# Optimization experiments

Measured on AMD Instinct MI355X. Metric: run time of the kernel, lower is better.

## Reference

```python
import jax, jax.numpy as jnp
import numpy as np


def setup_inputs() -> dict:
    key = jax.random.key(0)
    ks = jax.random.split(key, 5)
    B, S, D = 2, 2048, 1024
    inv = 1.0 / np.sqrt(D)
    inp = {
        "x": jax.random.normal(ks[0], (B, S, D), jnp.float32),
        "Wq": jax.random.normal(ks[1], (D, D), jnp.float32) * inv,
        "bq": jnp.zeros((D,), jnp.float32),
        "Wk": jax.random.normal(ks[2], (D, D), jnp.float32) * inv,
        "bk": jnp.zeros((D,), jnp.float32),
        "Wv": jax.random.normal(ks[3], (D, D), jnp.float32) * inv,
        "bv": jnp.zeros((D,), jnp.float32),
        "Wo": jax.random.normal(ks[4], (D, D), jnp.float32) * inv,
        "bo": jnp.zeros((D,), jnp.float32),
        "num_heads": 16,
        "window_size": 128,
    }
    return inp


def reference(x, Wq, bq, Wk, bk, Wv, bv, Wo, bo, num_heads, window_size):
    B, S, D = x.shape
    H = num_heads
    hd = D // H
    scale = 1.0 / np.sqrt(hd)

    def split_heads(t):  # [B,S,D] -> [B,H,S,hd]
        return t.reshape(B, S, H, hd).transpose(0, 2, 1, 3)

    q = split_heads(x @ Wq + bq)
    k = split_heads(x @ Wk + bk)
    v = split_heads(x @ Wv + bv)

    # dense scores, then sliding-window + causal mask (faithful to original)
    scores = jnp.einsum('bhqd,bhkd->bhqk', q, k) * scale  # [B,H,S,S]
    i = jnp.arange(S)[:, None]
    j = jnp.arange(S)[None, :]
    # position i attends to j in [i - window_size + 1, i]
    mask = (j <= i) & (j > i - window_size)
    scores = jnp.where(mask, scores, -jnp.inf)
    attn_weights = jax.nn.softmax(scores, axis=-1)  # dropout is identity in eval

    out = jnp.einsum('bhqk,bhkd->bhqd', attn_weights, v)  # [B,H,S,hd]
    out = out.transpose(0, 2, 1, 3).reshape(B, S, D)
    return out @ Wo + bo, attn_weights
```

## Files before the change

kernel.cpp:

```cpp
#include <hip/hip_runtime.h>
#include <cmath>

typedef __attribute__((ext_vector_type(8))) __bf16 v8bf;
typedef __attribute__((ext_vector_type(4))) float  v4f;

#define DEV static __device__ __forceinline__

DEV unsigned short f2bf(float f) {
  unsigned u = __builtin_bit_cast(unsigned, f);
  unsigned r = u + 0x7fffu + ((u >> 16) & 1u);
  return (unsigned short)(r >> 16);
}
DEV float bf2f(unsigned short s) {
  return __builtin_bit_cast(float, ((unsigned)s) << 16);
}
DEV v8bf ld8(const unsigned short* p) { return *(const v8bf*)p; }

DEV void gl16(const unsigned short* g, unsigned short* l) {
  __builtin_amdgcn_global_load_lds(
      (const __attribute__((address_space(1))) unsigned int*)g,
      (__attribute__((address_space(3))) unsigned int*)l, 16, 0, 0);
}

__global__ __launch_bounds__(256) void k_cvt_x(const float* __restrict__ x,
                                               unsigned short* __restrict__ xb) {
  int i = blockIdx.x * 256 + threadIdx.x;
  float4 v = ((const float4*)x)[i];
  unsigned lo = (unsigned)f2bf(v.x) | ((unsigned)f2bf(v.y) << 16);
  unsigned hi = (unsigned)f2bf(v.z) | ((unsigned)f2bf(v.w) << 16);
  ((uint2*)xb)[i] = make_uint2(lo, hi);
}

__global__ __launch_bounds__(256) void k_trans_w4(const float* __restrict__ Wq,
                                                  const float* __restrict__ Wk,
                                                  const float* __restrict__ Wv,
                                                  const float* __restrict__ Wo,
                                                  unsigned short* __restrict__ WT,
                                                  unsigned short* __restrict__ WoT) {
  __shared__ float t[32][33];
  int z = blockIdx.z;
  const float* src = (z == 0) ? Wq : (z == 1) ? Wk : (z == 2) ? Wv : Wo;
  unsigned short* dst = (z < 3) ? WT + z * 1048576 : WoT;
  int n0 = blockIdx.x * 32, k0 = blockIdx.y * 32;
  int tx = threadIdx.x & 31, ty = threadIdx.x >> 5;
  for (int r = ty; r < 32; r += 8)
    t[r][tx] = src[(k0 + r) * 1024 + n0 + tx];
  __syncthreads();
  for (int r = ty; r < 32; r += 8)
    dst[(n0 + r) * 1024 + k0 + tx] = f2bf(t[tx][r]);
}

__global__ __launch_bounds__(256) void k_bias(const float* __restrict__ bq,
                                              const float* __restrict__ bk,
                                              const float* __restrict__ bv,
                                              float* __restrict__ dst) {
  int i = blockIdx.x * 256 + threadIdx.x;
  float v = (i < 1024) ? bq[i] : (i < 2048 ? bk[i - 1024] : bv[i - 2048]);
  dst[i] = v;
}

template <bool OUT_F32>
__global__ __launch_bounds__(256) void k_gemm(const unsigned short* __restrict__ A,
                                              const unsigned short* __restrict__ Bt,
                                              const float* __restrict__ bias,
                                              void* __restrict__ Cout,
                                              int ldc) {
  constexpr int K = 1024;
  __shared__ __attribute__((aligned(16))) unsigned short As[128 * 32];
  __shared__ __attribute__((aligned(16))) unsigned short Bs[128 * 32];
  int tid = threadIdx.x;
  int wave = tid >> 6, lane = tid & 63;
  int m0 = blockIdx.y * 128, n0 = blockIdx.x * 128;
  int wm = (wave >> 1) * 64, wn = (wave & 1) * 64;
  int m = lane & 15, q4 = lane >> 4;
  int arow = tid >> 2, acol = (tid & 3) * 8;
  v4f acc[4][4] = {};
  const unsigned short* ga0 = A + (m0 + arow) * K + acol;
  const unsigned short* ga1 = A + (m0 + 64 + arow) * K + acol;
  const unsigned short* gb0 = Bt + (n0 + arow) * K + acol;
  const unsigned short* gb1 = Bt + (n0 + 64 + arow) * K + acol;
  unsigned short* lA0 = As + wave * 512;
  unsigned short* lA1 = As + 2048 + wave * 512;
  unsigned short* lB0 = Bs + wave * 512;
  unsigned short* lB1 = Bs + 2048 + wave * 512;

  for (int kt = 0; kt < K; kt += 32) {
    gl16(ga0 + kt, lA0);
    gl16(ga1 + kt, lA1);
    gl16(gb0 + kt, lB0);
    gl16(gb1 + kt, lB1);
    __syncthreads();
    v8bf af[4], bfv[4];
#pragma unroll
    for (int mt = 0; mt < 4; mt++) af[mt] = ld8(&As[(wm + mt * 16 + m) * 32 + q4 * 8]);
#pragma unroll
    for (int nt = 0; nt < 4; nt++) bfv[nt] = ld8(&Bs[(wn + nt * 16 + m) * 32 + q4 * 8]);
#pragma unroll
    for (int mt = 0; mt < 4; mt++)
#pragma unroll
      for (int nt = 0; nt < 4; nt++)
        acc[mt][nt] = __builtin_amdgcn_mfma_f32_16x16x32_bf16(af[mt], bfv[nt], acc[mt][nt], 0, 0, 0);
    __syncthreads();
  }
#pragma unroll
  for (int mt = 0; mt < 4; mt++)
#pragma unroll
    for (int nt = 0; nt < 4; nt++) {
      int col = n0 + wn + nt * 16 + m;
      float bb = bias[col];
#pragma unroll
      for (int r = 0; r < 4; r++) {
        int row = m0 + wm + mt * 16 + q4 * 4 + r;
        float v = acc[mt][nt][r] + bb;
        if (OUT_F32) ((float*)Cout)[row * ldc + col] = v;
        else ((unsigned short*)Cout)[row * ldc + col] = f2bf(v);
      }
    }
}

__global__ __launch_bounds__(256) void k_attn(const unsigned short* __restrict__ QKV,
                                              unsigned short* __restrict__ Oatt,
                                              unsigned short* __restrict__ cb) {
  constexpr int VTS = 208;
  constexpr int PSS = 168;
  __shared__ __attribute__((aligned(16))) unsigned short Vt[64 * VTS];
  __shared__ __attribute__((aligned(16))) unsigned short Ps[4][16 * PSS];
  int b = blockIdx.z, h = blockIdx.y, i0 = blockIdx.x * 64;
  int tid = threadIdx.x, wave = tid >> 6, lane = tid & 63;
  int kbase = i0 - 128;
  const int ld = 3072;
  const unsigned short* Qg = QKV + b * 2048 * ld + h * 64;
  const unsigned short* Kg = Qg + 1024;
  const unsigned short* Vg = Qg + 2048;

  for (int c = tid; c < 192 * 16; c += 256) {
    int jl = c & 15, rest = c >> 4;
    int d0 = (rest & 15) * 4;
    int j = (rest >> 4) * 16 + jl;
    int jg = kbase + j; jg = jg < 0 ? 0 : jg;
    uint2 v = *(const uint2*)(Vg + jg * ld + d0);
    Vt[(d0 + 0) * VTS + j] = (unsigned short)(v.x & 0xffffu);
    Vt[(d0 + 1) * VTS + j] = (unsigned short)(v.x >> 16);
    Vt[(d0 + 2) * VTS + j] = (unsigned short)(v.y & 0xffffu);
    Vt[(d0 + 3) * VTS + j] = (unsigned short)(v.y >> 16);
  }
  for (int c = tid; c < 64 * 16; c += 256)
    Vt[(c >> 4) * VTS + 192 + (c & 15)] = 0;
  for (int c = lane; c < 16 * 24; c += 64)
    Ps[wave][(c / 24) * PSS + 144 + (c % 24)] = 0;
  __syncthreads();

  int qb = i0 + wave * 16;
  int m = lane & 15, q4 = lane >> 4;

  const unsigned short* qrow = Qg + (qb + m) * ld;
  v8bf qa0 = ld8(qrow + q4 * 8);
  v8bf qa1 = ld8(qrow + 32 + q4 * 8);

  v4f sc[9];
#pragma unroll
  for (int n = 0; n < 9; n++) {
    int key = kbase + wave * 16 + n * 16 + m;
    int kg = key < 0 ? 0 : key;
    const unsigned short* krow = Kg + kg * ld;
    v8bf kb0 = ld8(krow + q4 * 8);
    v8bf kb1 = ld8(krow + 32 + q4 * 8);
    v4f z = {0.f, 0.f, 0.f, 0.f};
    z = __builtin_amdgcn_mfma_f32_16x16x32_bf16(qa0, kb0, z, 0, 0, 0);
    z = __builtin_amdgcn_mfma_f32_16x16x32_bf16(qa1, kb1, z, 0, 0, 0);
    sc[n] = z;
  }
  float mx[4] = {-3e38f, -3e38f, -3e38f, -3e38f};
#pragma unroll
  for (int n = 0; n < 9; n++)
#pragma unroll
    for (int r = 0; r < 4; r++) {
      int i = qb + q4 * 4 + r;
      int j = kbase + wave * 16 + n * 16 + m;
      float v = sc[n][r] * 0.125f;
      bool ok = (j >= 0) && (j <= i) && (j > i - 128);
      v = ok ? v : -3e38f;
      sc[n][r] = v;
      mx[r] = fmaxf(mx[r], v);
    }
#pragma unroll
  for (int o = 1; o < 16; o <<= 1)
#pragma unroll
    for (int r = 0; r < 4; r++) mx[r] = fmaxf(mx[r], __shfl_xor(mx[r], o, 64));
  float sum[4] = {0.f, 0.f, 0.f, 0.f};
#pragma unroll
  for (int n = 0; n < 9; n++)
#pragma unroll
    for (int r = 0; r < 4; r++) {
      float p = __expf(sc[n][r] - mx[r]);
      sc[n][r] = p;
      sum[r] += p;
    }
#pragma unroll
  for (int o = 1; o < 16; o <<= 1)
#pragma unroll
    for (int r = 0; r < 4; r++) sum[r] += __shfl_xor(sum[r], o, 64);
  float inv[4];
#pragma unroll
  for (int r = 0; r < 4; r++) inv[r] = 1.0f / sum[r];

#pragma unroll
  for (int n = 0; n < 9; n++)
#pragma unroll
    for (int r = 0; r < 4; r++)
      Ps[wave][(q4 * 4 + r) * PSS + n * 16 + m] = f2bf(sc[n][r] * inv[r]);
  __syncthreads();

  v4f oacc[4] = {};
#pragma unroll
  for (int c = 0; c < 5; c++) {
    v8bf pa = ld8(&Ps[wave][m * PSS + c * 32 + q4 * 8]);
#pragma unroll
    for (int dt = 0; dt < 4; dt++) {
      v8bf vb = ld8(&Vt[(dt * 16 + m) * VTS + wave * 16 + c * 32 + q4 * 8]);
      oacc[dt] = __builtin_amdgcn_mfma_f32_16x16x32_bf16(pa, vb, oacc[dt], 0, 0, 0);
    }
  }
#pragma unroll
  for (int dt = 0; dt < 4; dt++)
#pragma unroll
    for (int r = 0; r < 4; r++)
      Oatt[(b * 2048 + qb + q4 * 4 + r) * 1024 + h * 64 + dt * 16 + m] = f2bf(oacc[dt][r]);

  for (int R = 0; R < 16; R++) {
    int row = (b * 16 + h) * 2048 + qb + R;
    unsigned short p0 = Ps[wave][R * PSS + R + 1 + lane * 2];
    unsigned short p1 = Ps[wave][R * PSS + R + 2 + lane * 2];
    ((unsigned*)cb)[row * 64 + lane] = (unsigned)p0 | ((unsigned)p1 << 16);
  }
}

__global__ __launch_bounds__(256) void k_wwrite(const unsigned short* __restrict__ cb,
                                                float* __restrict__ wout) {
  int tid = threadIdx.x, wave = tid >> 6, lane = tid & 63;
  int rbase = blockIdx.x * 16 + wave * 4;
  for (int rr = 0; rr < 4; rr++) {
    int row = rbase + rr;
    int i = row & 2047;
    float* rowp = wout + (size_t)row * 2048;
    const unsigned short* crow = cb + (size_t)row * 128;
    int lo = i - 127;
#pragma unroll
    for (int it = 0; it < 8; it++) {
      int col = it * 256 + lane * 4;
      float4 v = {0.f, 0.f, 0.f, 0.f};
      if (col <= i && col + 3 >= lo) {
#pragma unroll
        for (int e = 0; e < 4; e++) {
          int j = col + e;
          if (j >= lo && j <= i && j >= 0)
            (&v.x)[e] = bf2f(crow[j - lo]);
        }
      }
      *(float4*)(rowp + col) = v;
    }
  }
}

extern "C" void kernel_launch(void* const* d_in, const int* in_sizes, int n_in,
                              void* d_out, int out_size, void* d_ws, size_t ws_size,
                              hipStream_t stream) {
  (void)in_sizes; (void)n_in; (void)out_size; (void)ws_size;
  const float* x  = (const float*)d_in[0];
  const float* Wq = (const float*)d_in[1];
  const float* bq = (const float*)d_in[2];
  const float* Wk = (const float*)d_in[3];
  const float* bk = (const float*)d_in[4];
  const float* Wv = (const float*)d_in[5];
  const float* bv = (const float*)d_in[6];
  const float* Wo = (const float*)d_in[7];
  const float* bo = (const float*)d_in[8];

  char* ws = (char*)d_ws;
  unsigned short* xb   = (unsigned short*)(ws);
  unsigned short* WT   = (unsigned short*)(ws + 8388608);
  unsigned short* WoT  = (unsigned short*)(ws + 14680064);
  float*          bqkv = (float*)(ws + 16777216);
  unsigned short* QKV  = (unsigned short*)(ws + 16789504);
  unsigned short* Oat  = (unsigned short*)(ws + 41955328);
  unsigned short* cb   = (unsigned short*)(ws + 50343936);

  float* out  = (float*)d_out;
  float* wout = out + 4194304;

  k_cvt_x<<<4096, 256, 0, stream>>>(x, xb);
  k_trans_w4<<<dim3(32, 32, 4), 256, 0, stream>>>(Wq, Wk, Wv, Wo, WT, WoT);
  k_bias<<<12, 256, 0, stream>>>(bq, bk, bv, bqkv);
  k_gemm<false><<<dim3(24, 32), 256, 0, stream>>>(xb, WT, bqkv, QKV, 3072);
  k_attn<<<dim3(32, 16, 2), 256, 0, stream>>>(QKV, Oat, cb);
  k_wwrite<<<4096, 256, 0, stream>>>(cb, wout);
  k_gemm<true><<<dim3(8, 32), 256, 0, stream>>>(Oat, WoT, bo, out, 1024);
}
```

Before: 686.5 us.

## Merge prep kernels, pretranspose V globally, fuse out-proj GEMM with weight write

Folds the three preprocessing kernels into one launch and merges the output-projection GEMM with the attention-weights expansion kernel, so those independent jobs share one grid. Adds a separate kernel that transposes V into a global head-major buffer, letting the attention kernel fill its shared V tile with 16-byte vector loads instead of scattered 2-byte stores. Weight-matrix stores become nontemporal. The cost is an extra pass over V through global memory and an extra launch for the transpose.

```diff
diff --git a/kernel.cpp b/kernel.cpp
--- a/kernel.cpp
+++ b/kernel.cpp
@@ -22,49 +22,49 @@
       (__attribute__((address_space(3))) unsigned int*)l, 16, 0, 0);
 }
 
-__global__ __launch_bounds__(256) void k_cvt_x(const float* __restrict__ x,
-                                               unsigned short* __restrict__ xb) {
-  int i = blockIdx.x * 256 + threadIdx.x;
-  float4 v = ((const float4*)x)[i];
-  unsigned lo = (unsigned)f2bf(v.x) | ((unsigned)f2bf(v.y) << 16);
-  unsigned hi = (unsigned)f2bf(v.z) | ((unsigned)f2bf(v.w) << 16);
-  ((uint2*)xb)[i] = make_uint2(lo, hi);
-}
-
-__global__ __launch_bounds__(256) void k_trans_w4(const float* __restrict__ Wq,
-                                                  const float* __restrict__ Wk,
-                                                  const float* __restrict__ Wv,
-                                                  const float* __restrict__ Wo,
-                                                  unsigned short* __restrict__ WT,
-                                                  unsigned short* __restrict__ WoT) {
-  __shared__ float t[32][33];
-  int z = blockIdx.z;
-  const float* src = (z == 0) ? Wq : (z == 1) ? Wk : (z == 2) ? Wv : Wo;
-  unsigned short* dst = (z < 3) ? WT + z * 1048576 : WoT;
-  int n0 = blockIdx.x * 32, k0 = blockIdx.y * 32;
-  int tx = threadIdx.x & 31, ty = threadIdx.x >> 5;
-  for (int r = ty; r < 32; r += 8)
-    t[r][tx] = src[(k0 + r) * 1024 + n0 + tx];
-  __syncthreads();
-  for (int r = ty; r < 32; r += 8)
-    dst[(n0 + r) * 1024 + k0 + tx] = f2bf(t[tx][r]);
-}
-
-__global__ __launch_bounds__(256) void k_bias(const float* __restrict__ bq,
+__global__ __launch_bounds__(256) void k_prep(const float* __restrict__ x,
+                                              const float* __restrict__ Wq,
+                                              const float* __restrict__ Wk,
+                                              const float* __restrict__ Wv,
+                                              const float* __restrict__ Wo,
+                                              const float* __restrict__ bq,
                                               const float* __restrict__ bk,
                                               const float* __restrict__ bv,
-                                              float* __restrict__ dst) {
-  int i = blockIdx.x * 256 + threadIdx.x;
-  float v = (i < 1024) ? bq[i] : (i < 2048 ? bk[i - 1024] : bv[i - 2048]);
-  dst[i] = v;
-}
-
-template <bool OUT_F32>
-__global__ __launch_bounds__(256) void k_gemm(const unsigned short* __restrict__ A,
-                                              const unsigned short* __restrict__ Bt,
-                                              const float* __restrict__ bias,
-                                              void* __restrict__ Cout,
-                                              int ldc) {
+                                              unsigned short* __restrict__ xb,
+                                              unsigned short* __restrict__ WT,
+                                              unsigned short* __restrict__ WoT,
+                                              float* __restrict__ bqkv) {
+  __shared__ float t[32][33];
+  int bx = blockIdx.x, tid = threadIdx.x;
+  if (bx < 4096) {
+    int i = bx * 256 + tid;
+    float4 v = ((const float4*)x)[i];
+    unsigned lo = (unsigned)f2bf(v.x) | ((unsigned)f2bf(v.y) << 16);
+    unsigned hi = (unsigned)f2bf(v.z) | ((unsigned)f2bf(v.w) << 16);
+    ((uint2*)xb)[i] = make_uint2(lo, hi);
+  } else if (bx < 8192) {
+    int rem = bx - 4096;
+    int z = rem >> 10, r2 = rem & 1023;
+    const float* src = (z == 0) ? Wq : (z == 1) ? Wk : (z == 2) ? Wv : Wo;
+    unsigned short* dst = (z < 3) ? WT + z * 1048576 : WoT;
+    int n0 = (r2 & 31) * 32, k0 = (r2 >> 5) * 32;
+    int tx = tid & 31, ty = tid >> 5;
+    for (int r = ty; r < 32; r += 8)
+      t[r][tx] = src[(k0 + r) * 1024 + n0 + tx];
+    __syncthreads();
+    for (int r = ty; r < 32; r += 8)
+      dst[(n0 + r) * 1024 + k0 + tx] = f2bf(t[tx][r]);
+  } else {
+    int i = (bx - 8192) * 256 + tid;
+    float v = (i < 1024) ? bq[i] : (i < 2048 ? bk[i - 1024] : bv[i - 2048]);
+    bqkv[i] = v;
+  }
+}
+
+__global__ __launch_bounds__(256) void k_gemm1(const unsigned short* __restrict__ A,
+                                               const unsigned short* __restrict__ Bt,
+                                               const float* __restrict__ bias,
+                                               unsigned short* __restrict__ Cout) {
   constexpr int K = 1024;
   __shared__ __attribute__((aligned(16))) unsigned short As[128 * 32];
   __shared__ __attribute__((aligned(16))) unsigned short Bs[128 * 32];
@@ -111,14 +111,30 @@
 #pragma unroll
       for (int r = 0; r < 4; r++) {
         int row = m0 + wm + mt * 16 + q4 * 4 + r;
-        float v = acc[mt][nt][r] + bb;
-        if (OUT_F32) ((float*)Cout)[row * ldc + col] = v;
-        else ((unsigned short*)Cout)[row * ldc + col] = f2bf(v);
+        Cout[row * 3072 + col] = f2bf(acc[mt][nt][r] + bb);
       }
     }
 }
 
+__global__ __launch_bounds__(256) void k_transv(const unsigned short* __restrict__ QKV,
+                                                unsigned short* __restrict__ Vtg) {
+  __shared__ unsigned short t[32][33];
+  int bx = blockIdx.x, tid = threadIdx.x;
+  int st = bx & 63, h2 = (bx >> 6) & 1, bh = bx >> 7;
+  int b = bh >> 4, h = bh & 15;
+  int s0 = st * 32, d0 = h2 * 32;
+  int tx = tid & 31, ty = tid >> 5;
+  const unsigned short* src = QKV + (size_t)b * 2048 * 3072 + 2048 + h * 64 + d0;
+  for (int r = ty; r < 32; r += 8)
+    t[r][tx] = src[(size_t)(s0 + r) * 3072 + tx];
+  __syncthreads();
+  unsigned short* dst = Vtg + (size_t)(bh * 64 + d0) * 2048 + s0;
+  for (int r = ty; r < 32; r += 8)
+    dst[(size_t)r * 2048 + tx] = t[tx][r];
+}
+
 __global__ __launch_bounds__(256) void k_attn(const unsigned short* __restrict__ QKV,
+                                              const unsigned short* __restrict__ Vtg,
                                               unsigned short* __restrict__ Oatt,
                                               unsigned short* __restrict__ cb) {
   constexpr int VTS = 208;
@@ -131,21 +147,19 @@
   const int ld = 3072;
   const unsigned short* Qg = QKV + b * 2048 * ld + h * 64;
   const unsigned short* Kg = Qg + 1024;
-  const unsigned short* Vg = Qg + 2048;
-
-  for (int c = tid; c < 192 * 16; c += 256) {
-    int jl = c & 15, rest = c >> 4;
-    int d0 = (rest & 15) * 4;
-    int j = (rest >> 4) * 16 + jl;
-    int jg = kbase + j; jg = jg < 0 ? 0 : jg;
-    uint2 v = *(const uint2*)(Vg + jg * ld + d0);
-    Vt[(d0 + 0) * VTS + j] = (unsigned short)(v.x & 0xffffu);
-    Vt[(d0 + 1) * VTS + j] = (unsigned short)(v.x >> 16);
-    Vt[(d0 + 2) * VTS + j] = (unsigned short)(v.y & 0xffffu);
-    Vt[(d0 + 3) * VTS + j] = (unsigned short)(v.y >> 16);
-  }
-  for (int c = tid; c < 64 * 16; c += 256)
-    Vt[(c >> 4) * VTS + 192 + (c & 15)] = 0;
+
+  const unsigned short* vsrc = Vtg + (size_t)(b * 16 + h) * 64 * 2048;
+  for (int idx = tid; idx < 1536; idx += 256) {
+    int row = idx / 24, c16 = idx % 24;
+    int gcol = kbase + c16 * 8;
+    if (gcol < 0) gcol = 0;
+    v8bf vv = ld8(vsrc + (size_t)row * 2048 + gcol);
+    *(v8bf*)&Vt[row * VTS + c16 * 8] = vv;
+  }
+  {
+    int row = tid >> 2, c4 = (tid & 3) * 4;
+    *(uint2*)&Vt[row * VTS + 192 + c4] = make_uint2(0u, 0u);
+  }
   for (int c = lane; c < 16 * 24; c += 64)
     Ps[wave][(c / 24) * PSS + 144 + (c % 24)] = 0;
   __syncthreads();
@@ -235,29 +249,85 @@
   }
 }
 
-__global__ __launch_bounds__(256) void k_wwrite(const unsigned short* __restrict__ cb,
-                                                float* __restrict__ wout) {
+__global__ __launch_bounds__(256) void k_tail(const unsigned short* __restrict__ Oat,
+                                              const unsigned short* __restrict__ WoT,
+                                              const float* __restrict__ bo,
+                                              float* __restrict__ out,
+                                              const unsigned short* __restrict__ cb,
+                                              float* __restrict__ wout) {
+  __shared__ __attribute__((aligned(16))) unsigned short As[128 * 32];
+  __shared__ __attribute__((aligned(16))) unsigned short Bs[128 * 32];
   int tid = threadIdx.x, wave = tid >> 6, lane = tid & 63;
-  int rbase = blockIdx.x * 16 + wave * 4;
-  for (int rr = 0; rr < 4; rr++) {
-    int row = rbase + rr;
-    int i = row & 2047;
-    float* rowp = wout + (size_t)row * 2048;
-    const unsigned short* crow = cb + (size_t)row * 128;
-    int lo = i - 127;
-#pragma unroll
-    for (int it = 0; it < 8; it++) {
-      int col = it * 256 + lane * 4;
-      float4 v = {0.f, 0.f, 0.f, 0.f};
-      if (col <= i && col + 3 >= lo) {
-#pragma unroll
-        for (int e = 0; e < 4; e++) {
-          int j = col + e;
-          if (j >= lo && j <= i && j >= 0)
-            (&v.x)[e] = bf2f(crow[j - lo]);
+
+  if (blockIdx.x < 256) {
+    constexpr int K = 1024;
+    int bx = blockIdx.x;
+    int n0 = (bx & 7) * 128, m0 = (bx >> 3) * 128;
+    int wm = (wave >> 1) * 64, wn = (wave & 1) * 64;
+    int m = lane & 15, q4 = lane >> 4;
+    int arow = tid >> 2, acol = (tid & 3) * 8;
+    v4f acc[4][4] = {};
+    const unsigned short* ga0 = Oat + (m0 + arow) * K + acol;
+    const unsigned short* ga1 = Oat + (m0 + 64 + arow) * K + acol;
+    const unsigned short* gb0 = WoT + (n0 + arow) * K + acol;
+    const unsigned short* gb1 = WoT + (n0 + 64 + arow) * K + acol;
+    unsigned short* lA0 = As + wave * 512;
+    unsigned short* lA1 = As + 2048 + wave * 512;
+    unsigned short* lB0 = Bs + wave * 512;
+    unsigned short* lB1 = Bs + 2048 + wave * 512;
+    for (int kt = 0; kt < K; kt += 32) {
+      gl16(ga0 + kt, lA0);
+      gl16(ga1 + kt, lA1);
+      gl16(gb0 + kt, lB0);
+      gl16(gb1 + kt, lB1);
+      __syncthreads();
+      v8bf af[4], bfv[4];
+#pragma unroll
+      for (int mt = 0; mt < 4; mt++) af[mt] = ld8(&As[(wm + mt * 16 + m) * 32 + q4 * 8]);
+#pragma unroll
+      for (int nt = 0; nt < 4; nt++) bfv[nt] = ld8(&Bs[(wn + nt * 16 + m) * 32 + q4 * 8]);
+#pragma unroll
+      for (int mt = 0; mt < 4; mt++)
+#pragma unroll
+        for (int nt = 0; nt < 4; nt++)
+          acc[mt][nt] = __builtin_amdgcn_mfma_f32_16x16x32_bf16(af[mt], bfv[nt], acc[mt][nt], 0, 0, 0);
+      __syncthreads();
+    }
+#pragma unroll
+    for (int mt = 0; mt < 4; mt++)
+#pragma unroll
+      for (int nt = 0; nt < 4; nt++) {
+        int col = n0 + wn + nt * 16 + m;
+        float bb = bo[col];
+#pragma unroll
+        for (int r = 0; r < 4; r++) {
+          int row = m0 + wm + mt * 16 + q4 * 4 + r;
+          out[row * 1024 + col] = acc[mt][nt][r] + bb;
         }
       }
-      *(float4*)(rowp + col) = v;
+  } else {
+    int wb = blockIdx.x - 256;
+    int rbase = wb * 16 + wave * 4;
+    for (int rr = 0; rr < 4; rr++) {
+      int row = rbase + rr;
+      int i = row & 2047;
+      float* rowp = wout + (size_t)row * 2048;
+      const unsigned short* crow = cb + (size_t)row * 128;
+      int lo = i - 127;
+#pragma unroll
+      for (int it = 0; it < 8; it++) {
+        int col = it * 256 + lane * 4;
+        v4f v = {0.f, 0.f, 0.f, 0.f};
+        if (col <= i && col + 3 >= lo) {
+#pragma unroll
+          for (int e = 0; e < 4; e++) {
+            int j = col + e;
+            if (j >= lo && j <= i && j >= 0)
+              v[e] = bf2f(crow[j - lo]);
+          }
+        }
+        __builtin_nontemporal_store(v, (v4f*)(rowp + col));
+      }
     }
   }
 }
@@ -284,15 +354,14 @@
   unsigned short* QKV  = (unsigned short*)(ws + 16789504);
   unsigned short* Oat  = (unsigned short*)(ws + 41955328);
   unsigned short* cb   = (unsigned short*)(ws + 50343936);
+  unsigned short* Vtg  = (unsigned short*)(ws + 67121152);
 
   float* out  = (float*)d_out;
   float* wout = out + 4194304;
 
-  k_cvt_x<<<4096, 256, 0, stream>>>(x, xb);
-  k_trans_w4<<<dim3(32, 32, 4), 256, 0, stream>>>(Wq, Wk, Wv, Wo, WT, WoT);
-  k_bias<<<12, 256, 0, stream>>>(bq, bk, bv, bqkv);
-  k_gemm<false><<<dim3(24, 32), 256, 0, stream>>>(xb, WT, bqkv, QKV, 3072);
-  k_attn<<<dim3(32, 16, 2), 256, 0, stream>>>(QKV, Oat, cb);
-  k_wwrite<<<4096, 256, 0, stream>>>(cb, wout);
-  k_gemm<true><<<dim3(8, 32), 256, 0, stream>>>(Oat, WoT, bo, out, 1024);
-}
+  k_prep<<<8204, 256, 0, stream>>>(x, Wq, Wk, Wv, Wo, bq, bk, bv, xb, WT, WoT, bqkv);
+  k_gemm1<<<dim3(24, 32), 256, 0, stream>>>(xb, WT, bqkv, QKV);
+  k_transv<<<4096, 256, 0, stream>>>(QKV, Vtg);
+  k_attn<<<dim3(32, 16, 2), 256, 0, stream>>>(QKV, Vtg, Oat, cb);
+  k_tail<<<4352, 256, 0, stream>>>(Oat, WoT, bo, out, cb, wout);
+}
```

New measurement: 641.6 us. 6.5% less time.
